# Kernel tuning notes

Measured on AMD Instinct MI355X. Metric: run time of the kernel, lower is better.

## Reference

```python
import jax, jax.numpy as jnp
import numpy as np
from jax import lax

DIM = 192
WS = 8
NH = 6


def setup_inputs() -> dict:
    key = jax.random.key(0)
    ks = jax.random.split(key, 7)
    B, H, W, C = 8, 128, 128, DIM
    s = 1.0 / np.sqrt(C)
    x = jax.random.normal(ks[0], (B, H, W, C), dtype=jnp.float32)
    w_qkv = jax.random.normal(ks[1], (C, 3 * C), dtype=jnp.float32) * s
    b_qkv = jnp.zeros((3 * C,), dtype=jnp.float32)
    # depthwise 3x3 conv kernel in HWIO layout with feature_group_count=C -> (3,3,1,C)
    w_dw = jax.random.normal(ks[2], (3, 3, 1, C), dtype=jnp.float32) * (1.0 / 3.0)
    b_dw = jnp.zeros((C,), dtype=jnp.float32)
    w_proj = jax.random.normal(ks[3], (C, C), dtype=jnp.float32) * s
    b_proj = jnp.zeros((C,), dtype=jnp.float32)
    return {"x": x, "w_qkv": w_qkv, "b_qkv": b_qkv, "w_dw": w_dw,
            "b_dw": b_dw, "w_proj": w_proj, "b_proj": b_proj}


def reference(x, w_qkv, b_qkv, w_dw, b_dw, w_proj, b_proj):
    B, H, W, C = x.shape
    hd = C // NH
    # qkv projection: [B,H,W,3C]
    qkv = x @ w_qkv + b_qkv
    # window partition: (3, B*nWh*nWw*NH, WS*WS, hd)
    qkv = qkv.reshape(B, H // WS, WS, W // WS, WS, 3, NH, hd)
    qkv = qkv.transpose(5, 0, 1, 3, 6, 2, 4, 7).reshape(3, -1, WS * WS, hd)
    q, k, v = qkv[0], qkv[1], qkv[2]
    q = q * (hd ** -0.5)
    attn = jax.nn.softmax(jnp.einsum('wik,wjk->wij', q, k), axis=-1)
    o = jnp.einsum('wij,wjk->wik', attn, v)
    # window reverse -> [B,H,W,C]
    o = o.reshape(B, H // WS, W // WS, NH, WS, WS, hd)
    o = o.transpose(0, 1, 4, 2, 5, 3, 6).reshape(B, H, W, C)
    # proj tail: depthwise 3x3 conv (pad=1) then linear
    o = lax.conv_general_dilated(o, w_dw, window_strides=(1, 1),
                                 padding=[(1, 1), (1, 1)],
                                 dimension_numbers=('NHWC', 'HWIO', 'NHWC'),
                                 feature_group_count=C) + b_dw
    o = o @ w_proj + b_proj
    return o
```

## Files before the change

### kernel.cpp

```cpp
#include <hip/hip_runtime.h>


typedef __attribute__((ext_vector_type(8))) short bf16x8;
typedef __attribute__((ext_vector_type(4))) float f32x4;

__device__ __forceinline__ float bf2f(unsigned short h) {
    return __builtin_bit_cast(float, (unsigned int)h << 16);
}
__device__ __forceinline__ unsigned short f2bf(float f) {
    unsigned int u = __builtin_bit_cast(unsigned int, f);
    u += 0x7fffu + ((u >> 16) & 1u);
    return (unsigned short)(u >> 16);
}
__device__ __forceinline__ bf16x8 ld8(const unsigned short* p) {
    return *(const bf16x8*)p;
}
__device__ __forceinline__ bf16x8 ldf8(const float* p) {
    float4 a = *(const float4*)p;
    float4 b = *(const float4*)(p + 4);
    bf16x8 r;
    r[0] = (short)f2bf(a.x); r[1] = (short)f2bf(a.y);
    r[2] = (short)f2bf(a.z); r[3] = (short)f2bf(a.w);
    r[4] = (short)f2bf(b.x); r[5] = (short)f2bf(b.y);
    r[6] = (short)f2bf(b.z); r[7] = (short)f2bf(b.w);
    return r;
}

__global__ __launch_bounds__(256) void repack_kernel(
    const float* __restrict__ w_qkv, const float* __restrict__ w_proj,
    unsigned short* __restrict__ wq_m, unsigned short* __restrict__ wp_m)
{
    int f = blockIdx.x * 256 + threadIdx.x;
    if (f < 6 * 36 * 64 * 8) {
        int j = f & 7, lane = (f >> 3) & 63, rest = f >> 9;
        int nt = rest % 36, kt = rest / 36;
        wq_m[f] = f2bf(w_qkv[(kt * 32 + (lane >> 4) * 8 + j) * 576 + nt * 16 + (lane & 15)]);
    }
    if (f < 6 * 12 * 64 * 8) {
        int j = f & 7, lane = (f >> 3) & 63, rest = f >> 9;
        int nt = rest % 12, kt = rest / 12;
        wp_m[f] = f2bf(w_proj[(kt * 32 + (lane >> 4) * 8 + j) * 192 + nt * 16 + (lane & 15)]);
    }
}

__global__ __launch_bounds__(384) void qkv_attn_fused(
    const float* __restrict__ x, const unsigned short* __restrict__ wq_m,
    const float* __restrict__ b_qkv, unsigned short* __restrict__ o_scr)
{
    __shared__ unsigned short smem[12800 + 6 * 7424];

    const int tid = threadIdx.x, lane = tid & 63, h = tid >> 6;
    const int l16 = lane & 15, quad = lane >> 4;
    const int wi = blockIdx.x;
    const int img = wi >> 8, wrem = wi & 255;
    const int y0 = (wrem >> 4) * 8, x0 = (wrem & 15) * 8;

    {
        const int token = tid / 6, seg = tid % 6;
        const float* sp = x + ((img * 128 + y0 + (token >> 3)) * 128
                               + (x0 + (token & 7))) * 192 + seg * 32;
        unsigned short* dp = smem + token * 200 + seg * 32;
#pragma unroll
        for (int i = 0; i < 4; ++i)
            *(bf16x8*)(dp + i * 8) = ldf8(sp + i * 8);
    }
    __syncthreads();

    unsigned short* qs = smem + 12800 + h * 7424;
    unsigned short* ks = qs + 2560;
    unsigned short* vT = qs + 5120;
    unsigned short* Ps = qs;

    const int ntb[6] = {2 * h, 2 * h + 1, 12 + 2 * h, 13 + 2 * h, 24 + 2 * h, 25 + 2 * h};

    f32x4 acc[6][4];
#pragma unroll
    for (int s = 0; s < 6; ++s)
#pragma unroll
        for (int mt = 0; mt < 4; ++mt) acc[s][mt] = (f32x4){0.f, 0.f, 0.f, 0.f};

    for (int kt = 0; kt < 6; ++kt) {
        bf16x8 af[4];
#pragma unroll
        for (int mt = 0; mt < 4; ++mt)
            af[mt] = ld8(smem + (mt * 16 + l16) * 200 + kt * 32 + quad * 8);
#pragma unroll
        for (int s = 0; s < 6; ++s) {
            bf16x8 bw = ld8(wq_m + (((kt * 36 + ntb[s]) * 64 + lane) << 3));
#pragma unroll
            for (int mt = 0; mt < 4; ++mt)
                acc[s][mt] = __builtin_amdgcn_mfma_f32_16x16x32_bf16(af[mt], bw, acc[s][mt], 0, 0, 0);
        }
    }

#pragma unroll
    for (int s = 0; s < 6; ++s) {
        const float bias = b_qkv[ntb[s] * 16 + l16];
        if (s < 2) {
#pragma unroll
            for (int mt = 0; mt < 4; ++mt)
#pragma unroll
                for (int r = 0; r < 4; ++r)
                    qs[(mt * 16 + quad * 4 + r) * 40 + s * 16 + l16] =
                        f2bf((acc[s][mt][r] + bias) * 0.17677669529663687f);
        } else if (s < 4) {
#pragma unroll
            for (int mt = 0; mt < 4; ++mt)
#pragma unroll
                for (int r = 0; r < 4; ++r)
                    ks[(mt * 16 + quad * 4 + r) * 40 + (s - 2) * 16 + l16] =
                        f2bf(acc[s][mt][r] + bias);
        } else {
#pragma unroll
            for (int mt = 0; mt < 4; ++mt)
#pragma unroll
                for (int r = 0; r < 4; ++r)
                    vT[((s - 4) * 16 + l16) * 72 + mt * 16 + quad * 4 + r] =
                        f2bf(acc[s][mt][r] + bias);
        }
    }

    bf16x8 aq[4], bk[4];
#pragma unroll
    for (int mt = 0; mt < 4; ++mt) aq[mt] = ld8(qs + (mt * 16 + l16) * 40 + quad * 8);
#pragma unroll
    for (int nt = 0; nt < 4; ++nt) bk[nt] = ld8(ks + (nt * 16 + l16) * 40 + quad * 8);

    f32x4 s4[4][4];
#pragma unroll
    for (int mt = 0; mt < 4; ++mt)
#pragma unroll
        for (int nt = 0; nt < 4; ++nt) {
            s4[mt][nt] = (f32x4){0.f, 0.f, 0.f, 0.f};
            s4[mt][nt] = __builtin_amdgcn_mfma_f32_16x16x32_bf16(aq[mt], bk[nt], s4[mt][nt], 0, 0, 0);
        }

#pragma unroll
    for (int mt = 0; mt < 4; ++mt) {
#pragma unroll
        for (int r = 0; r < 4; ++r) {
            float m = fmaxf(fmaxf(s4[mt][0][r], s4[mt][1][r]), fmaxf(s4[mt][2][r], s4[mt][3][r]));
            m = fmaxf(m, __shfl_xor(m, 1, 64));
            m = fmaxf(m, __shfl_xor(m, 2, 64));
            m = fmaxf(m, __shfl_xor(m, 4, 64));
            m = fmaxf(m, __shfl_xor(m, 8, 64));
            float pv[4], sum = 0.f;
#pragma unroll
            for (int nt = 0; nt < 4; ++nt) { pv[nt] = __expf(s4[mt][nt][r] - m); sum += pv[nt]; }
            sum += __shfl_xor(sum, 1, 64);
            sum += __shfl_xor(sum, 2, 64);
            sum += __shfl_xor(sum, 4, 64);
            sum += __shfl_xor(sum, 8, 64);
            const float inv = 1.f / sum;
            const int row = mt * 16 + quad * 4 + r;
#pragma unroll
            for (int nt = 0; nt < 4; ++nt)
                Ps[row * 72 + nt * 16 + l16] = f2bf(pv[nt] * inv);
        }
    }

    f32x4 o[4][2];
#pragma unroll
    for (int mt = 0; mt < 4; ++mt)
#pragma unroll
        for (int n2 = 0; n2 < 2; ++n2) o[mt][n2] = (f32x4){0.f, 0.f, 0.f, 0.f};

#pragma unroll
    for (int kt2 = 0; kt2 < 2; ++kt2) {
        bf16x8 bv[2];
#pragma unroll
        for (int n2 = 0; n2 < 2; ++n2)
            bv[n2] = ld8(vT + (n2 * 16 + l16) * 72 + kt2 * 32 + quad * 8);
#pragma unroll
        for (int mt = 0; mt < 4; ++mt) {
            bf16x8 ap = ld8(Ps + (mt * 16 + l16) * 72 + kt2 * 32 + quad * 8);
#pragma unroll
            for (int n2 = 0; n2 < 2; ++n2)
                o[mt][n2] = __builtin_amdgcn_mfma_f32_16x16x32_bf16(ap, bv[n2], o[mt][n2], 0, 0, 0);
        }
    }

#pragma unroll
    for (int mt = 0; mt < 4; ++mt)
#pragma unroll
        for (int n2 = 0; n2 < 2; ++n2)
#pragma unroll
            for (int r = 0; r < 4; ++r) {
                const int token = mt * 16 + quad * 4 + r;
                o_scr[((img * 128 + y0 + (token >> 3)) * 128 + (x0 + (token & 7))) * 192
                      + h * 32 + n2 * 16 + l16] = f2bf(o[mt][n2][r]);
            }
}

__global__ __launch_bounds__(256, 2) void conv_proj_kernel(
    const unsigned short* __restrict__ o_scr,
    const float* __restrict__ w_dw, const float* __restrict__ b_dw,
    const unsigned short* __restrict__ wp_m, const float* __restrict__ b_proj,
    float* __restrict__ out)
{
    __shared__ unsigned short oh[100 * 192];
    __shared__ unsigned short cb[64 * 200];
    __shared__ float wdw_s[9 * 192];
    __shared__ float bdw_s[192];

    const int tid = threadIdx.x, lane = tid & 63, wave = tid >> 6;
    const int l16 = lane & 15, quad = lane >> 4;
    const int img = blockIdx.x >> 8, wrem = blockIdx.x & 255;
    const int y0 = (wrem >> 4) * 8, x0 = (wrem & 15) * 8;

    for (int i = tid; i < 9 * 192; i += 256) wdw_s[i] = w_dw[i];
    if (tid < 192) bdw_s[tid] = b_dw[tid];

    for (int c = tid; c < 2400; c += 256) {
        int pix = c / 24, ck = c % 24;
        int py = y0 - 1 + pix / 10, px = x0 - 1 + pix % 10;
        uint4 v = {0u, 0u, 0u, 0u};
        if (py >= 0 && py < 128 && px >= 0 && px < 128)
            v = *(const uint4*)(o_scr + ((img * 128 + py) * 128 + px) * 192 + ck * 8);
        *(uint4*)(oh + pix * 192 + ck * 8) = v;
    }
    __syncthreads();

#pragma unroll
    for (int k = 0; k < 6; ++k) {
        int idx = k * 256 + tid;
        int c8 = idx % 24, t = idx / 24;
        int r = t >> 3, cc = t & 7;
        float a[8];
#pragma unroll
        for (int i = 0; i < 8; ++i) a[i] = bdw_s[c8 * 8 + i];
#pragma unroll
        for (int dy = 0; dy < 3; ++dy)
#pragma unroll
            for (int dx = 0; dx < 3; ++dx) {
                bf16x8 hv = ld8(&oh[((r + dy) * 10 + (cc + dx)) * 192 + c8 * 8]);
                const float* wp = &wdw_s[(dy * 3 + dx) * 192 + c8 * 8];
#pragma unroll
                for (int i = 0; i < 8; ++i)
                    a[i] += bf2f((unsigned short)hv[i]) * wp[i];
            }
        bf16x8 rv;
#pragma unroll
        for (int i = 0; i < 8; ++i) rv[i] = (short)f2bf(a[i]);
        *(bf16x8*)&cb[t * 200 + c8 * 8] = rv;
    }
    __syncthreads();

    f32x4 po[3][4];
#pragma unroll
    for (int n = 0; n < 3; ++n)
#pragma unroll
        for (int mt = 0; mt < 4; ++mt) po[n][mt] = (f32x4){0.f, 0.f, 0.f, 0.f};

    for (int kt = 0; kt < 6; ++kt) {
        bf16x8 af[4];
#pragma unroll
        for (int mt = 0; mt < 4; ++mt) af[mt] = ld8(cb + (mt * 16 + l16) * 200 + kt * 32 + quad * 8);
#pragma unroll
        for (int ntl = 0; ntl < 3; ++ntl) {
            bf16x8 bw = ld8(wp_m + (((kt * 12 + wave * 3 + ntl) * 64 + lane) << 3));
#pragma unroll
            for (int mt = 0; mt < 4; ++mt)
                po[ntl][mt] = __builtin_amdgcn_mfma_f32_16x16x32_bf16(af[mt], bw, po[ntl][mt], 0, 0, 0);
        }
    }

#pragma unroll
    for (int ntl = 0; ntl < 3; ++ntl) {
        int col = (wave * 3 + ntl) * 16 + l16;
        float bias = b_proj[col];
#pragma unroll
        for (int mt = 0; mt < 4; ++mt)
#pragma unroll
            for (int r = 0; r < 4; ++r) {
                int t = mt * 16 + quad * 4 + r;
                out[((img * 128 + y0 + (t >> 3)) * 128 + (x0 + (t & 7))) * 192 + col]
                    = po[ntl][mt][r] + bias;
            }
    }
}

extern "C" void kernel_launch(void* const* d_in, const int* in_sizes, int n_in,
                              void* d_out, int out_size, void* d_ws, size_t ws_size,
                              hipStream_t stream)
{
    const float* x      = (const float*)d_in[0];
    const float* w_qkv  = (const float*)d_in[1];
    const float* b_qkv  = (const float*)d_in[2];
    const float* w_dw   = (const float*)d_in[3];
    const float* b_dw   = (const float*)d_in[4];
    const float* w_proj = (const float*)d_in[5];
    const float* b_proj = (const float*)d_in[6];
    float* out = (float*)d_out;

    unsigned short* wq_m  = (unsigned short*)d_ws;
    unsigned short* wp_m  = wq_m + 110592;
    unsigned short* o_scr = wq_m + 147456;

    repack_kernel<<<dim3(432), dim3(256), 0, stream>>>(w_qkv, w_proj, wq_m, wp_m);
    qkv_attn_fused<<<dim3(2048), dim3(384), 0, stream>>>(x, wq_m, b_qkv, o_scr);
    conv_proj_kernel<<<dim3(2048), dim3(256), 0, stream>>>(o_scr, w_dw, b_dw, wp_m, b_proj, out);
}
```

Before: 313.4 us.

## Drop shared x staging, load x directly per wave, and swizzle attention LDS

Each wave now reads its x fragments straight from global memory, converting them to bf16 in registers, instead of first staging the whole window tile in shared memory behind a barrier. The per-head Q/K/V/P buffers shrink to a packed 64-wide layout with an XOR swizzle to avoid bank conflicts, which cuts the LDS footprint so that three blocks can be resident per CU. The cost is that x is now loaded redundantly from global memory by all six head waves rather than once per block.

```diff
diff --git a/kernel.cpp b/kernel.cpp
--- a/kernel.cpp
+++ b/kernel.cpp
@@ -43,11 +43,11 @@
     }
 }
 
-__global__ __launch_bounds__(384) void qkv_attn_fused(
+__global__ __launch_bounds__(384, 3) void qkv_attn_fused(
     const float* __restrict__ x, const unsigned short* __restrict__ wq_m,
     const float* __restrict__ b_qkv, unsigned short* __restrict__ o_scr)
 {
-    __shared__ unsigned short smem[12800 + 6 * 7424];
+    __shared__ unsigned short smem[6 * 6144];
 
     const int tid = threadIdx.x, lane = tid & 63, h = tid >> 6;
     const int l16 = lane & 15, quad = lane >> 4;
@@ -55,21 +55,15 @@
     const int img = wi >> 8, wrem = wi & 255;
     const int y0 = (wrem >> 4) * 8, x0 = (wrem & 15) * 8;
 
-    {
-        const int token = tid / 6, seg = tid % 6;
-        const float* sp = x + ((img * 128 + y0 + (token >> 3)) * 128
-                               + (x0 + (token & 7))) * 192 + seg * 32;
-        unsigned short* dp = smem + token * 200 + seg * 32;
-#pragma unroll
-        for (int i = 0; i < 4; ++i)
-            *(bf16x8*)(dp + i * 8) = ldf8(sp + i * 8);
-    }
-    __syncthreads();
-
-    unsigned short* qs = smem + 12800 + h * 7424;
-    unsigned short* ks = qs + 2560;
-    unsigned short* vT = qs + 5120;
-    unsigned short* Ps = qs;
+    unsigned short* qk = smem + h * 6144;
+    unsigned short* vT = qk + 4096;
+
+    const float* xrow[4];
+#pragma unroll
+    for (int mt = 0; mt < 4; ++mt) {
+        int token = mt * 16 + l16;
+        xrow[mt] = x + ((img * 128 + y0 + (token >> 3)) * 128 + (x0 + (token & 7))) * 192;
+    }
 
     const int ntb[6] = {2 * h, 2 * h + 1, 12 + 2 * h, 13 + 2 * h, 24 + 2 * h, 25 + 2 * h};
 
@@ -82,8 +76,7 @@
     for (int kt = 0; kt < 6; ++kt) {
         bf16x8 af[4];
 #pragma unroll
-        for (int mt = 0; mt < 4; ++mt)
-            af[mt] = ld8(smem + (mt * 16 + l16) * 200 + kt * 32 + quad * 8);
+        for (int mt = 0; mt < 4; ++mt) af[mt] = ldf8(xrow[mt] + kt * 32 + quad * 8);
 #pragma unroll
         for (int s = 0; s < 6; ++s) {
             bf16x8 bw = ld8(wq_m + (((kt * 36 + ntb[s]) * 64 + lane) << 3));
@@ -96,35 +89,41 @@
 #pragma unroll
     for (int s = 0; s < 6; ++s) {
         const float bias = b_qkv[ntb[s] * 16 + l16];
-        if (s < 2) {
+        if (s < 4) {
+            const int c0 = s * 16 + l16;
+            const float scl = (s < 2) ? 0.17677669529663687f : 1.0f;
 #pragma unroll
             for (int mt = 0; mt < 4; ++mt)
 #pragma unroll
-                for (int r = 0; r < 4; ++r)
-                    qs[(mt * 16 + quad * 4 + r) * 40 + s * 16 + l16] =
-                        f2bf((acc[s][mt][r] + bias) * 0.17677669529663687f);
-        } else if (s < 4) {
+                for (int r = 0; r < 4; ++r) {
+                    const int row = mt * 16 + quad * 4 + r;
+                    qk[row * 64 + (c0 ^ ((row & 7) << 3))] =
+                        f2bf((acc[s][mt][r] + bias) * scl);
+                }
+        } else {
+            const int rowv = (s - 4) * 16 + l16;
+            const int sw = (rowv & 7) << 3;
 #pragma unroll
             for (int mt = 0; mt < 4; ++mt)
 #pragma unroll
-                for (int r = 0; r < 4; ++r)
-                    ks[(mt * 16 + quad * 4 + r) * 40 + (s - 2) * 16 + l16] =
-                        f2bf(acc[s][mt][r] + bias);
-        } else {
-#pragma unroll
-            for (int mt = 0; mt < 4; ++mt)
-#pragma unroll
-                for (int r = 0; r < 4; ++r)
-                    vT[((s - 4) * 16 + l16) * 72 + mt * 16 + quad * 4 + r] =
-                        f2bf(acc[s][mt][r] + bias);
+                for (int r = 0; r < 4; ++r) {
+                    const int tok = mt * 16 + quad * 4 + r;
+                    vT[rowv * 64 + (tok ^ sw)] = f2bf(acc[s][mt][r] + bias);
+                }
         }
     }
 
     bf16x8 aq[4], bk[4];
 #pragma unroll
-    for (int mt = 0; mt < 4; ++mt) aq[mt] = ld8(qs + (mt * 16 + l16) * 40 + quad * 8);
-#pragma unroll
-    for (int nt = 0; nt < 4; ++nt) bk[nt] = ld8(ks + (nt * 16 + l16) * 40 + quad * 8);
+    for (int mt = 0; mt < 4; ++mt) {
+        const int row = mt * 16 + l16;
+        aq[mt] = ld8(qk + row * 64 + ((quad * 8) ^ ((row & 7) << 3)));
+    }
+#pragma unroll
+    for (int nt = 0; nt < 4; ++nt) {
+        const int row = nt * 16 + l16;
+        bk[nt] = ld8(qk + row * 64 + ((32 + quad * 8) ^ ((row & 7) << 3)));
+    }
 
     f32x4 s4[4][4];
 #pragma unroll
@@ -153,9 +152,10 @@
             sum += __shfl_xor(sum, 8, 64);
             const float inv = 1.f / sum;
             const int row = mt * 16 + quad * 4 + r;
+            const int sw = (row & 7) << 3;
 #pragma unroll
             for (int nt = 0; nt < 4; ++nt)
-                Ps[row * 72 + nt * 16 + l16] = f2bf(pv[nt] * inv);
+                qk[row * 64 + ((nt * 16 + l16) ^ sw)] = f2bf(pv[nt] * inv);
         }
     }
 
@@ -169,11 +169,14 @@
     for (int kt2 = 0; kt2 < 2; ++kt2) {
         bf16x8 bv[2];
 #pragma unroll
-        for (int n2 = 0; n2 < 2; ++n2)
-            bv[n2] = ld8(vT + (n2 * 16 + l16) * 72 + kt2 * 32 + quad * 8);
+        for (int n2 = 0; n2 < 2; ++n2) {
+            const int row = n2 * 16 + l16;
+            bv[n2] = ld8(vT + row * 64 + ((kt2 * 32 + quad * 8) ^ ((row & 7) << 3)));
+        }
 #pragma unroll
         for (int mt = 0; mt < 4; ++mt) {
-            bf16x8 ap = ld8(Ps + (mt * 16 + l16) * 72 + kt2 * 32 + quad * 8);
+            const int row = mt * 16 + l16;
+            bf16x8 ap = ld8(qk + row * 64 + ((kt2 * 32 + quad * 8) ^ ((row & 7) << 3)));
 #pragma unroll
             for (int n2 = 0; n2 < 2; ++n2)
                 o[mt][n2] = __builtin_amdgcn_mfma_f32_16x16x32_bf16(ap, bv[n2], o[mt][n2], 0, 0, 0);
```

After: 382.0 us. +21.9%, slower.
